# Kernel tuning notes

Hardware: AMD Instinct MI355X
Metric: run time of the kernel (lower is better)

## Reference

```python
import jax, jax.numpy as jnp
import numpy as np
import itertools
from jax import lax

KERNEL_LENGTH = 9
DILATION = 4
ALPHA = -1.0
BETA = 2.0
PADDING = (KERNEL_LENGTH - 1) * DILATION // 2  # 16, keeps T constant


def make_weights():
    # torch.combinations(arange(9), 3) enumerates index triples in lexicographic order;
    # each kernel is alpha everywhere with beta at the 3 chosen positions -> 84 kernels.
    combs = list(itertools.combinations(range(KERNEL_LENGTH), KERNEL_LENGTH // 3))
    w = np.full((len(combs), 1, KERNEL_LENGTH), ALPHA, dtype=np.float32)
    for i, c in enumerate(combs):
        w[i, 0, list(c)] = BETA
    return jnp.asarray(w)  # (K=84, 1, 9)


def setup_inputs() -> dict:
    key = jax.random.key(0)
    x = jax.random.normal(key, (16, 16, 4096), dtype=jnp.float32)  # (B, C, T)
    return {"x": x}


def reference(x) -> jnp.ndarray:
    w = make_weights()  # (K, 1, 9) fixed ternary kernels (non-trainable buffer)
    B, C, T = x.shape
    K = w.shape[0]
    # Depthwise: every input channel is convolved with all K kernels independently.
    # Fold (B, C) into the batch dim so a single grouped-free conv suffices.
    xr = x.reshape(B * C, 1, T)
    y = lax.conv_general_dilated(
        xr, w,
        window_strides=(1,),
        padding=[(PADDING, PADDING)],
        rhs_dilation=(DILATION,),
        dimension_numbers=("NCH", "OIH", "NCH"),
    )  # (B*C, K, T)
    # Match torch: conv output channel order is (channel-group, kernel); the module
    # then views it as (B, K, C, T). Replicate the identical reshape semantics.
    y = y.reshape(B, C * K, T).reshape(B, K, C, T)
    return y
```

## Files before the change

### kernel.cpp

```cpp
#include <hip/hip_runtime.h>


#define KLEN 9
#define NK   84
#define BB   16
#define CC   16
#define TT   4096
#define TILE 1024
#define HALO 16
#define LDS_N (TILE + 2 * HALO)

struct CombTable { int a[NK], b[NK], c[NK]; };
constexpr CombTable make_combs() {
    CombTable t{};
    int n = 0;
    for (int i = 0; i < KLEN; ++i)
        for (int j = i + 1; j < KLEN; ++j)
            for (int k = j + 1; k < KLEN; ++k) {
                t.a[n] = i; t.b[n] = j; t.c[n] = k; ++n;
            }
    return t;
}
constexpr CombTable COMBS = make_combs();

__global__ __launch_bounds__(256) void rocket_conv(const float* __restrict__ x,
                                                   float* __restrict__ out) {
    __shared__ __align__(16) float lds[LDS_N];

    const int tid  = threadIdx.x;
    const int tile = blockIdx.x;
    const int c    = blockIdx.y;
    const int b    = blockIdx.z;
    const int t0   = tile * TILE;

    const float* xbc = x + ((size_t)b * CC + c) * TT;
    for (int i = tid; i < LDS_N; i += 256) {
        int g = t0 - HALO + i;
        lds[i] = (g >= 0 && g < TT) ? xbc[g] : 0.0f;
    }
    __syncthreads();

    const int lt = 4 * tid;
    float4 tap[KLEN];
#pragma unroll
    for (int j = 0; j < KLEN; ++j)
        tap[j] = *(const float4*)&lds[lt + 4 * j];

    float4 s;
    s.x = s.y = s.z = s.w = 0.0f;
#pragma unroll
    for (int j = 0; j < KLEN; ++j) {
        s.x += tap[j].x; s.y += tap[j].y; s.z += tap[j].z; s.w += tap[j].w;
    }

    float4* o = (float4*)out +
                (((size_t)(b * CC + c) * NK) * TT + t0 + lt) / 4;
    const size_t kstr = TT / 4;

#pragma unroll
    for (int k = 0; k < NK; ++k) {
        const float4 ta = tap[COMBS.a[k]];
        const float4 tb = tap[COMBS.b[k]];
        const float4 tc = tap[COMBS.c[k]];
        float4 r;
        r.x = 3.0f * (ta.x + tb.x + tc.x) - s.x;
        r.y = 3.0f * (ta.y + tb.y + tc.y) - s.y;
        r.z = 3.0f * (ta.z + tb.z + tc.z) - s.z;
        r.w = 3.0f * (ta.w + tb.w + tc.w) - s.w;
        o[(size_t)k * kstr] = r;
    }
}

extern "C" void kernel_launch(void* const* d_in, const int* in_sizes, int n_in,
                              void* d_out, int out_size, void* d_ws, size_t ws_size,
                              hipStream_t stream) {
    const float* x = (const float*)d_in[0];
    float* out     = (float*)d_out;
    dim3 grid(TT / TILE, CC, BB);
    rocket_conv<<<grid, 256, 0, stream>>>(x, out);
}
```

Measured before the change: 343.7 us.

## Split blocks by kernel groups, load full row, use nontemporal stores

Each block now covers a whole 4096-sample row and a quarter of the 84 kernels, instead of a 1024-sample time tile with all kernels. Threads process two float4 groups each, and outputs are written with nontemporal stores, which bypass cache for the large write stream of about 88 MB. The trade-offs are that each input row is now loaded by four blocks, register pressure rises, and a switch dispatches to templated compile-time comb indices.

```diff
diff --git a/kernel.cpp b/kernel.cpp
--- a/kernel.cpp
+++ b/kernel.cpp
@@ -6,9 +6,13 @@
 #define BB   16
 #define CC   16
 #define TT   4096
-#define TILE 1024
 #define HALO 16
-#define LDS_N (TILE + 2 * HALO)
+#define KG   4
+#define KPB  (NK / KG)
+#define NTHR 512
+#define LDS_N (TT + 2 * HALO)
+
+typedef float f4 __attribute__((ext_vector_type(4)));
 
 struct CombTable { int a[NK], b[NK], c[NK]; };
 constexpr CombTable make_combs() {
@@ -23,59 +27,71 @@
 }
 constexpr CombTable COMBS = make_combs();
 
-__global__ __launch_bounds__(256) void rocket_conv(const float* __restrict__ x,
-                                                   float* __restrict__ out) {
+template <int K0>
+__device__ __forceinline__ void emit_rows(const f4 (&tap)[2][KLEN],
+                                          const f4 (&s)[2],
+                                          float* __restrict__ obase) {
+#pragma unroll
+    for (int n = 0; n < KPB; ++n) {
+        const int ia = COMBS.a[K0 + n];
+        const int ib = COMBS.b[K0 + n];
+        const int ic = COMBS.c[K0 + n];
+#pragma unroll
+        for (int g = 0; g < 2; ++g) {
+            f4 r = (tap[g][ia] + tap[g][ib] + tap[g][ic]) * 3.0f - s[g];
+            __builtin_nontemporal_store(
+                r, (f4*)(obase + (size_t)n * TT + g * (NTHR * 4)));
+        }
+    }
+}
+
+__global__ __launch_bounds__(NTHR) void rocket_conv(const float* __restrict__ x,
+                                                    float* __restrict__ out) {
     __shared__ __align__(16) float lds[LDS_N];
 
-    const int tid  = threadIdx.x;
-    const int tile = blockIdx.x;
-    const int c    = blockIdx.y;
-    const int b    = blockIdx.z;
-    const int t0   = tile * TILE;
+    const int tid = threadIdx.x;
+    const int kg  = blockIdx.x;
+    const int c   = blockIdx.y;
+    const int b   = blockIdx.z;
 
     const float* xbc = x + ((size_t)b * CC + c) * TT;
-    for (int i = tid; i < LDS_N; i += 256) {
-        int g = t0 - HALO + i;
-        lds[i] = (g >= 0 && g < TT) ? xbc[g] : 0.0f;
+    *(f4*)&lds[HALO + 4 * tid]          = *(const f4*)&xbc[4 * tid];
+    *(f4*)&lds[HALO + 4 * (tid + NTHR)] = *(const f4*)&xbc[4 * (tid + NTHR)];
+    if (tid < HALO) {
+        lds[tid] = 0.0f;
+        lds[HALO + TT + tid] = 0.0f;
     }
     __syncthreads();
 
-    const int lt = 4 * tid;
-    float4 tap[KLEN];
+    f4 tap[2][KLEN];
+    f4 s[2];
 #pragma unroll
-    for (int j = 0; j < KLEN; ++j)
-        tap[j] = *(const float4*)&lds[lt + 4 * j];
-
-    float4 s;
-    s.x = s.y = s.z = s.w = 0.0f;
+    for (int g = 0; g < 2; ++g) {
+        const int t0 = 4 * tid + (NTHR * 4) * g;
 #pragma unroll
-    for (int j = 0; j < KLEN; ++j) {
-        s.x += tap[j].x; s.y += tap[j].y; s.z += tap[j].z; s.w += tap[j].w;
+        for (int j = 0; j < KLEN; ++j) tap[g][j] = *(const f4*)&lds[t0 + 4 * j];
+        f4 acc = tap[g][0];
+#pragma unroll
+        for (int j = 1; j < KLEN; ++j) acc += tap[g][j];
+        s[g] = acc;
     }
 
-    float4* o = (float4*)out +
-                (((size_t)(b * CC + c) * NK) * TT + t0 + lt) / 4;
-    const size_t kstr = TT / 4;
-
-#pragma unroll
-    for (int k = 0; k < NK; ++k) {
-        const float4 ta = tap[COMBS.a[k]];
-        const float4 tb = tap[COMBS.b[k]];
-        const float4 tc = tap[COMBS.c[k]];
-        float4 r;
-        r.x = 3.0f * (ta.x + tb.x + tc.x) - s.x;
-        r.y = 3.0f * (ta.y + tb.y + tc.y) - s.y;
-        r.z = 3.0f * (ta.z + tb.z + tc.z) - s.z;
-        r.w = 3.0f * (ta.w + tb.w + tc.w) - s.w;
-        o[(size_t)k * kstr] = r;
+    float* obase = out + ((size_t)(b * CC + c) * NK + (size_t)kg * KPB) * TT
+                       + 4 * tid;
+    switch (kg & 3) {
+        case 0: emit_rows<0 * KPB>(tap, s, obase); break;
+        case 1: emit_rows<1 * KPB>(tap, s, obase); break;
+        case 2: emit_rows<2 * KPB>(tap, s, obase); break;
+        default: emit_rows<3 * KPB>(tap, s, obase); break;
     }
 }
 
 extern "C" void kernel_launch(void* const* d_in, const int* in_sizes, int n_in,
                               void* d_out, int out_size, void* d_ws, size_t ws_size,
                               hipStream_t stream) {
+    (void)in_sizes; (void)n_in; (void)d_ws; (void)ws_size; (void)out_size;
     const float* x = (const float*)d_in[0];
     float* out     = (float*)d_out;
-    dim3 grid(TT / TILE, CC, BB);
-    rocket_conv<<<grid, 256, 0, stream>>>(x, out);
+    dim3 grid(KG, CC, BB);
+    rocket_conv<<<grid, NTHR, 0, stream>>>(x, out);
 }
```

Measured after the change: 346.1 us. Within noise of the previous version (+0.7%).
